# Performance work log

Measured on AMD Instinct MI355X. Metric: run time of the kernel, lower is better.

## Reference

```python
import jax, jax.numpy as jnp
import numpy as np

B = 128          # graphs per batch
NPG = 512        # nodes per graph
N = B * NPG      # 65536 nodes
E = 262144       # edges, avg degree 4, intra-graph only
IN_FEATS = 128
EDGE_FEATS = 32
EMB = 64
HEADS = 4
HC = EMB * HEADS  # 256
L = 3


def setup_inputs():
    ki = iter(jax.random.split(jax.random.key(0), 64))

    def nrm(shape):
        return jax.random.normal(next(ki), shape, jnp.float32)

    def lin(fan_in, shape):
        return jax.random.uniform(next(ki), shape, jnp.float32, -1.0, 1.0) / np.float32(np.sqrt(fan_in))

    x = nrm((N, IN_FEATS))
    edge_attr = nrm((E, EDGE_FEATS))
    g = jnp.arange(E) // (E // B)  # each edge stays inside its graph
    src = g * NPG + jax.random.randint(next(ki), (E,), 0, NPG)
    dst = g * NPG + jax.random.randint(next(ki), (E,), 0, NPG)
    edge_index = jnp.stack([src, dst]).astype(jnp.int32)
    batch_index = (jnp.arange(N) // NPG).astype(jnp.int32)
    d = dict(x=x, edge_attr=edge_attr, edge_index=edge_index, batch_index=batch_index)
    d['Wq1'] = lin(IN_FEATS, (IN_FEATS, HC)); d['bq1'] = lin(IN_FEATS, (HC,))
    d['Wk1'] = lin(IN_FEATS, (IN_FEATS, HC)); d['bk1'] = lin(IN_FEATS, (HC,))
    d['Wv1'] = lin(IN_FEATS, (IN_FEATS, HC)); d['bv1'] = lin(IN_FEATS, (HC,))
    d['We1'] = lin(EDGE_FEATS, (EDGE_FEATS, HC))
    d['Wskip1'] = lin(IN_FEATS, (IN_FEATS, HC)); d['bskip1'] = lin(IN_FEATS, (HC,))
    d['Wbeta1'] = lin(3 * HC, (3 * HC,))
    d['Wt1'] = lin(HC, (HC, EMB)); d['bt1'] = lin(HC, (EMB,))
    d['bng1'] = jnp.ones((EMB,), jnp.float32); d['bnb1'] = jnp.zeros((EMB,), jnp.float32)
    d['Wq'] = lin(EMB, (L, EMB, HC)); d['bq'] = lin(EMB, (L, HC))
    d['Wk'] = lin(EMB, (L, EMB, HC)); d['bk'] = lin(EMB, (L, HC))
    d['Wv'] = lin(EMB, (L, EMB, HC)); d['bv'] = lin(EMB, (L, HC))
    d['We'] = lin(EDGE_FEATS, (L, EDGE_FEATS, HC))
    d['Wskip'] = lin(EMB, (L, EMB, HC)); d['bskip'] = lin(EMB, (L, HC))
    d['Wbeta'] = lin(3 * HC, (L, 3 * HC))
    d['Wt'] = lin(HC, (L, HC, EMB)); d['bt'] = lin(HC, (L, EMB))
    d['bng'] = jnp.ones((L, EMB), jnp.float32); d['bnb'] = jnp.zeros((L, EMB), jnp.float32)
    d['pw0'] = lin(EMB, (EMB,)); d['pw2'] = lin(EMB, (EMB,))
    return d


def _tconv(x, src, dst, eattr, emask, Wq, bq, Wk, bk, Wv, bv, We, Wskip, bskip, Wbeta, n):
    # PyG TransformerConv (concat=True, beta=True, edge_dim), dropout off (eval)
    q = (x @ Wq + bq).reshape(n, HEADS, EMB)
    k = (x @ Wk + bk).reshape(n, HEADS, EMB)
    v = (x @ Wv + bv).reshape(n, HEADS, EMB)
    e = (eattr @ We).reshape(-1, HEADS, EMB)
    alpha = jnp.einsum('ehc,ehc->eh', q[dst], k[src] + e) / (EMB ** 0.5)
    alpha = jnp.where(emask[:, None], alpha, -jnp.inf)
    m = jax.ops.segment_max(alpha, dst, num_segments=n)
    m = jnp.where(jnp.isfinite(m), m, 0.0)
    p = jnp.where(emask[:, None], jnp.exp(alpha - m[dst]), 0.0)
    den = jax.ops.segment_sum(p, dst, num_segments=n)
    p = p / jnp.maximum(den, 1e-16)[dst]
    out = jax.ops.segment_sum((v[src] + e) * p[:, :, None], dst, num_segments=n).reshape(n, HC)
    xr = x @ Wskip + bskip
    beta = jax.nn.sigmoid(jnp.concatenate([out, xr, out - xr], axis=-1) @ Wbeta)[:, None]
    return beta * xr + (1.0 - beta) * out


def _bn(x, g, b):
    mu = x.mean(0)
    var = jnp.mean((x - mu) ** 2, 0)
    return (x - mu) / jnp.sqrt(var + 1e-5) * g + b


def _topk(x, src, dst, emask, w, npg, k_keep):
    # PyG TopKPooling: score = tanh(x.w / |w|), keep top ratio per graph, scale kept x by score
    n_graphs = x.shape[0] // npg
    score = jnp.tanh((x @ w) / jnp.linalg.norm(w))
    sv, idx = jax.lax.top_k(score.reshape(n_graphs, npg), k_keep)
    perm = (idx + jnp.arange(n_graphs)[:, None] * npg).reshape(-1)
    x_new = x[perm] * sv.reshape(-1)[:, None]
    new_idx = jnp.full(n_graphs * npg, -1, jnp.int32).at[perm].set(
        jnp.arange(n_graphs * k_keep, dtype=jnp.int32))
    sn, dn = new_idx[src], new_idx[dst]
    valid = emask & (sn >= 0) & (dn >= 0)
    return x_new, jnp.where(valid, sn, 0), jnp.where(valid, dn, 0), valid


def _forward(x, edge_attr, edge_index, batch_index, Wq1, bq1, Wk1, bk1, Wv1, bv1,
             We1, Wskip1, bskip1, Wbeta1, Wt1, bt1, bng1, bnb1,
             Wq, bq, Wk, bk, Wv, bv, We, Wskip, bskip, Wbeta, Wt, bt, bng, bnb,
             pw0, pw2):
    src, dst = edge_index[0], edge_index[1]
    emask = jnp.ones(src.shape, dtype=bool)
    n = x.shape[0]
    npg = n // B
    x = _tconv(x, src, dst, edge_attr, emask, Wq1, bq1, Wk1, bk1, Wv1, bv1,
               We1, Wskip1, bskip1, Wbeta1, n)
    x = _bn(jax.nn.relu(x @ Wt1 + bt1), bng1, bnb1)
    pool_w = {0: pw0, 2: pw2}
    greps = []
    for i in range(L):
        x = _tconv(x, src, dst, edge_attr, emask, Wq[i], bq[i], Wk[i], bk[i], Wv[i], bv[i],
                   We[i], Wskip[i], bskip[i], Wbeta[i], n)
        x = _bn(jax.nn.relu(x @ Wt[i] + bt[i]), bng[i], bnb[i])
        if i % 3 == 0 or i == L - 1:  # pooling at layers 0 and 2
            k_keep = npg // 2
            x, src, dst, emask = _topk(x, src, dst, emask, pool_w[i], npg, k_keep)
            npg = k_keep
            n = B * npg
            batch = jnp.arange(n) // npg  # pooled nodes stay contiguous per graph
            gmax = jax.ops.segment_max(x, batch, num_segments=B)
            gmean = jax.ops.segment_sum(x, batch, num_segments=B) / npg
            greps.append(jnp.concatenate([gmax, gmean], axis=-1))
    return greps[0] + greps[1]


def reference(x, edge_attr, edge_index, batch_index, Wq1, bq1, Wk1, bk1, Wv1, bv1,
              We1, Wskip1, bskip1, Wbeta1, Wt1, bt1, bng1, bnb1,
              Wq, bq, Wk, bk, Wv, bv, We, Wskip, bskip, Wbeta, Wt, bt, bng, bnb,
              pw0, pw2):
    return _forward(x, edge_attr, edge_index, batch_index, Wq1, bq1, Wk1, bk1, Wv1, bv1,
                    We1, Wskip1, bskip1, Wbeta1, Wt1, bt1, bng1, bnb1,
                    Wq, bq, Wk, bk, Wv, bv, We, Wskip, bskip, Wbeta, Wt, bt, bng, bnb,
                    pw0, pw2)
```

## Files before the change

kernel.cpp:

```cpp
#include <hip/hip_runtime.h>
#include <hip/hip_bf16.h>

#define NGRAPH 128
#define NTOT   65536
#define NE     262144
#define EPG    2048
#define HC     256

typedef __hip_bfloat16 bf16;

__device__ __forceinline__ float4 f4fma(float a, float4 b, float4 c){
  return make_float4(fmaf(a,b.x,c.x), fmaf(a,b.y,c.y), fmaf(a,b.z,c.z), fmaf(a,b.w,c.w));
}
__device__ __forceinline__ float4 f4add(float4 a, float4 b){
  return make_float4(a.x+b.x, a.y+b.y, a.z+b.z, a.w+b.w);
}

template<int F>
__global__ __launch_bounds__(256)
void gemm_qkvs_kernel(const float* __restrict__ X,
                      const float* __restrict__ W0, const float* __restrict__ B0,
                      const float* __restrict__ W1, const float* __restrict__ B1,
                      const float* __restrict__ W2, const float* __restrict__ B2,
                      const float* __restrict__ W3, const float* __restrict__ B3,
                      float* __restrict__ Y, long ystride)
{
  const int s = blockIdx.y;
  const float* __restrict__ W = (s==0)?W0:(s==1)?W1:(s==2)?W2:W3;
  const float* __restrict__ Bb= (s==0)?B0:(s==1)?B1:(s==2)?B2:B3;
  float* __restrict__ Yo = Y + (long)s*ystride;

  __shared__ __align__(16) float XsT[F][36];
  const int tid  = threadIdx.x;
  const int tcol = tid & 63;
  const int trow = tid >> 6;
  const long r0 = (long)blockIdx.x * 32;
  for (int idx = tid; idx < 32*F; idx += 256){
    int r = idx / F;
    int f = idx - r*F;
    XsT[f][r] = X[(r0 + r)*F + f];
  }
  __syncthreads();
  float4 acc[8];
#pragma unroll
  for (int r = 0; r < 8; ++r) acc[r] = make_float4(0.f,0.f,0.f,0.f);
#pragma unroll 4
  for (int f = 0; f < F; ++f){
    float4 w = *(const float4*)(&W[f*HC + 4*tcol]);
    float xs[8];
    *(float4*)&xs[0] = *(const float4*)(&XsT[f][8*trow]);
    *(float4*)&xs[4] = *(const float4*)(&XsT[f][8*trow + 4]);
#pragma unroll
    for (int r = 0; r < 8; ++r) acc[r] = f4fma(xs[r], w, acc[r]);
  }
  float4 bb = *(const float4*)(&Bb[4*tcol]);
#pragma unroll
  for (int r = 0; r < 8; ++r)
    *(float4*)(&Yo[(r0 + 8*trow + r)*HC + 4*tcol]) = f4add(acc[r], bb);
}

__global__ void mcomb_kernel(const float* __restrict__ Wq,
                             const float* __restrict__ bq,
                             const float* __restrict__ We,
                             int F, float* __restrict__ M)
{
  int id = blockIdx.x*256 + threadIdx.x;
  if (id >= (F+1)*128) return;
  int g = id >> 7;
  int j = id & 127;
  int h = j >> 5, f = j & 31;
  const float* row = (g < F) ? (Wq + (long)g*HC) : bq;
  const float* wr  = We + (long)f*HC + h*64;
  float s = 0.f;
#pragma unroll
  for (int c = 0; c < 64; ++c) s = fmaf(row[h*64 + c], wr[c], s);
  M[id] = s;
}

template<int F>
__global__ __launch_bounds__(256)
void qwe_gemm_kernel(const float* __restrict__ X, const float* __restrict__ M,
                     float* __restrict__ qwe)
{
  __shared__ __align__(16) float XsT[F][68];
  const int tid  = threadIdx.x;
  const int tcol = tid & 31;
  const int trow = tid >> 5;
  const long r0 = (long)blockIdx.x * 64;
  for (int idx = tid; idx < 64*F; idx += 256){
    int r = idx / F;
    int f = idx - r*F;
    XsT[f][r] = X[(r0 + r)*F + f];
  }
  __syncthreads();
  float4 acc[8];
#pragma unroll
  for (int r = 0; r < 8; ++r) acc[r] = make_float4(0.f,0.f,0.f,0.f);
#pragma unroll 4
  for (int f = 0; f < F; ++f){
    float4 w = *(const float4*)(&M[f*128 + 4*tcol]);
    float xs[8];
    *(float4*)&xs[0] = *(const float4*)(&XsT[f][8*trow]);
    *(float4*)&xs[4] = *(const float4*)(&XsT[f][8*trow + 4]);
#pragma unroll
    for (int r = 0; r < 8; ++r) acc[r] = f4fma(xs[r], w, acc[r]);
  }
  float4 bb = *(const float4*)(&M[F*128 + 4*tcol]);
#pragma unroll
  for (int r = 0; r < 8; ++r)
    *(float4*)(&qwe[(r0 + 8*trow + r)*128 + 4*tcol]) = f4add(acc[r], bb);
}

__global__ __launch_bounds__(256)
void csr_build_kernel(const int* __restrict__ dstA, int npgLoc,
                      int* __restrict__ eids, int* __restrict__ rowptr,
                      int* __restrict__ deg)
{
  __shared__ int dloc[2048];
  __shared__ int ord[2048];
  __shared__ int cnt[512];
  __shared__ int base[512];
  const int g = blockIdx.x, tid = threadIdx.x;
  const int ebase = g*2048;
  const int nbase = g*npgLoc;
  for (int e = tid; e < 2048; e += 256){
    int d = dstA[ebase + e];
    dloc[e] = (d >= 0) ? (d - nbase) : -1;
  }
  for (int d = tid; d < npgLoc; d += 256) cnt[d] = 0;
  __syncthreads();
  for (int r = 0; r < 8; ++r){
    const int e = r*256 + tid;
    const int d = dloc[e];
    int rk = -1;
    if (d >= 0){
      rk = cnt[d];
      for (int u = r*256; u < e; ++u)
        rk += (dloc[u] == d);
    }
    ord[e] = rk;
    __syncthreads();
    if (d >= 0) atomicAdd(&cnt[d], 1);
    __syncthreads();
  }
  if (tid == 0){
    int run = 0;
    for (int d = 0; d < npgLoc; ++d){ base[d] = run; run += cnt[d]; }
  }
  __syncthreads();
  for (int e = tid; e < 2048; e += 256){
    int d = dloc[e];
    if (d >= 0) eids[ebase + base[d] + ord[e]] = ebase + e;
  }
  for (int d = tid; d < npgLoc; d += 256){
    rowptr[nbase + d] = ebase + base[d];
    deg   [nbase + d] = cnt[d];
  }
}

__global__ __launch_bounds__(256)
void attn_kernel(int nodeOff,
                 const float* q, const float* __restrict__ k,
                 const float* __restrict__ v, const float* __restrict__ skip,
                 const float* __restrict__ qwe,
                 const int* __restrict__ rowptr, const int* __restrict__ deg,
                 const int* __restrict__ eids, const int* __restrict__ srcA,
                 const float* __restrict__ EA, const float* __restrict__ We,
                 const float* __restrict__ Wb, float* xout)
{
  const int lane = threadIdx.x & 63;
  const int g16  = lane & 15;
  const int il   = blockIdx.x*4 + (threadIdx.x >> 6);
  const int i    = nodeOff + il;

  float4 q4  = *(const float4*)(&q[(long)il*HC + 4*lane]);
  float2 qw2 = *(const float2*)(&qwe[(long)il*128 + 2*lane]);

  const int p0 = rowptr[i];
  const int dg = deg[i];
  int e_l = 0, s_l = 0;
  if (lane < dg){ e_l = eids[p0 + lane]; s_l = srcA[e_l] - nodeOff; }

  float m = -__builtin_inff();
  float den = 0.f;
  float4 acc = make_float4(0.f,0.f,0.f,0.f);
  float2 wsum = make_float2(0.f,0.f);

  for (int t = 0; t < dg; ++t){
    int e, s;
    if (t < 64){ e = __shfl(e_l, t); s = __shfl(s_l, t); }
    else { e = eids[p0 + t]; s = srcA[e] - nodeOff; }
    float2 ea2 = *(const float2*)(&EA[(long)e*32 + 2*g16]);
    float4 k4  = *(const float4*)(&k[(long)s*HC + 4*lane]);
    float4 v4  = *(const float4*)(&v[(long)s*HC + 4*lane]);
    float part = q4.x*k4.x + q4.y*k4.y + q4.z*k4.z + q4.w*k4.w
               + qw2.x*ea2.x + qw2.y*ea2.y;
    part += __shfl_xor(part, 1);
    part += __shfl_xor(part, 2);
    part += __shfl_xor(part, 4);
    part += __shfl_xor(part, 8);
    float alpha = part * 0.125f;
    float nm  = fmaxf(m, alpha);
    float scl = __expf(m - nm);
    float p   = __expf(alpha - nm);
    den = den*scl + p;
    acc.x = fmaf(acc.x, scl, p*v4.x);
    acc.y = fmaf(acc.y, scl, p*v4.y);
    acc.z = fmaf(acc.z, scl, p*v4.z);
    acc.w = fmaf(acc.w, scl, p*v4.w);
    wsum.x = fmaf(wsum.x, scl, p*ea2.x);
    wsum.y = fmaf(wsum.y, scl, p*ea2.y);
    m = nm;
  }

  float4 ecorr = make_float4(0.f,0.f,0.f,0.f);
#pragma unroll
  for (int j = 0; j < 16; ++j){
    int srcl = (lane & 48) | j;
    float wx = __shfl(wsum.x, srcl);
    float wy = __shfl(wsum.y, srcl);
    float4 w0 = *(const float4*)(&We[(2*j)*HC + 4*lane]);
    float4 w1 = *(const float4*)(&We[(2*j+1)*HC + 4*lane]);
    ecorr = f4fma(wx, w0, ecorr);
    ecorr = f4fma(wy, w1, ecorr);
  }
  float inv = 1.f / fmaxf(den, 1e-16f);
  float4 o = make_float4((acc.x+ecorr.x)*inv, (acc.y+ecorr.y)*inv,
                         (acc.z+ecorr.z)*inv, (acc.w+ecorr.w)*inv);

  float4 xr  = *(const float4*)(&skip[(long)il*HC + 4*lane]);
  float4 wb1 = *(const float4*)(&Wb[4*lane]);
  float4 wb2 = *(const float4*)(&Wb[HC + 4*lane]);
  float4 wb3 = *(const float4*)(&Wb[2*HC + 4*lane]);
  float tp = o.x*wb1.x + o.y*wb1.y + o.z*wb1.z + o.w*wb1.w
           + xr.x*wb2.x + xr.y*wb2.y + xr.z*wb2.z + xr.w*wb2.w
           + (o.x-xr.x)*wb3.x + (o.y-xr.y)*wb3.y
           + (o.z-xr.z)*wb3.z + (o.w-xr.w)*wb3.w;
  tp += __shfl_xor(tp, 1);
  tp += __shfl_xor(tp, 2);
  tp += __shfl_xor(tp, 4);
  tp += __shfl_xor(tp, 8);
  tp += __shfl_xor(tp, 16);
  tp += __shfl_xor(tp, 32);
  float beta = 1.f / (1.f + __expf(-tp));
  float4 xo = make_float4(beta*xr.x + (1.f-beta)*o.x,
                          beta*xr.y + (1.f-beta)*o.y,
                          beta*xr.z + (1.f-beta)*o.z,
                          beta*xr.w + (1.f-beta)*o.w);
  *(float4*)(&xout[(long)il*HC + 4*lane]) = xo;
}

__global__ __launch_bounds__(256)
void gemm_wt_kernel(const float* __restrict__ Xa, const float* __restrict__ Wt,
                    const float* __restrict__ bt, float* __restrict__ y)
{
  __shared__ __align__(16) float XsT[64][132];
  const int tid  = threadIdx.x;
  const int tcol = tid & 15;
  const int trow = tid >> 4;
  const long r0 = (long)blockIdx.x * 128;
  float4 acc[8];
#pragma unroll
  for (int r = 0; r < 8; ++r) acc[r] = make_float4(0.f,0.f,0.f,0.f);
  for (int kc = 0; kc < 4; ++kc){
    for (int idx = tid; idx < 128*64; idx += 256){
      int r = idx >> 6;
      int f = idx & 63;
      XsT[f][r] = Xa[(r0 + r)*HC + kc*64 + f];
    }
    __syncthreads();
#pragma unroll 4
    for (int f = 0; f < 64; ++f){
      float4 w = *(const float4*)(&Wt[(kc*64 + f)*64 + 4*tcol]);
      float xs[8];
      *(float4*)&xs[0] = *(const float4*)(&XsT[f][8*trow]);
      *(float4*)&xs[4] = *(const float4*)(&XsT[f][8*trow + 4]);
#pragma unroll
      for (int r = 0; r < 8; ++r) acc[r] = f4fma(xs[r], w, acc[r]);
    }
    __syncthreads();
  }
  float4 bb = *(const float4*)(&bt[4*tcol]);
#pragma unroll
  for (int r = 0; r < 8; ++r){
    float4 o = f4add(acc[r], bb);
    o.x = fmaxf(o.x, 0.f); o.y = fmaxf(o.y, 0.f);
    o.z = fmaxf(o.z, 0.f); o.w = fmaxf(o.w, 0.f);
    *(float4*)(&y[(r0 + 8*trow + r)*64 + 4*tcol]) = o;
  }
}

__global__ __launch_bounds__(256)
void bn_stats_kernel(const float* __restrict__ y, long total4,
                     float* __restrict__ psum, float* __restrict__ psq)
{
  __shared__ float s1[256][4], s2[256][4];
  const int tid = threadIdx.x;
  float a0=0,a1=0,a2=0,a3=0,b0=0,b1=0,b2=0,b3=0;
  const float4* y4 = (const float4*)y;
  for (long j = (long)blockIdx.x*256 + tid; j < total4; j += 65536){
    float4 v = y4[j];
    a0 += v.x; b0 += v.x*v.x;
    a1 += v.y; b1 += v.y*v.y;
    a2 += v.z; b2 += v.z*v.z;
    a3 += v.w; b3 += v.w*v.w;
  }
  s1[tid][0]=a0; s1[tid][1]=a1; s1[tid][2]=a2; s1[tid][3]=a3;
  s2[tid][0]=b0; s2[tid][1]=b1; s2[tid][2]=b2; s2[tid][3]=b3;
  __syncthreads();
  if (tid < 64){
    int t0 = tid >> 2, comp = tid & 3;
    float sa = 0.f, sb = 0.f;
#pragma unroll
    for (int kk = 0; kk < 16; ++kk){
      sa += s1[t0 + 16*kk][comp];
      sb += s2[t0 + 16*kk][comp];
    }
    psum[(long)blockIdx.x*64 + tid] = sa;
    psq [(long)blockIdx.x*64 + tid] = sb;
  }
}

__global__ void bn_finalize_kernel(const float* __restrict__ psum,
                                   const float* __restrict__ psq,
                                   float n_f, float* musd)
{
  __shared__ float s1[4][64], s2[4][64];
  const int col = threadIdx.x & 63;
  const int part = threadIdx.x >> 6;
  float a = 0.f, b = 0.f;
  for (int j = part; j < 256; j += 4){
    a += psum[(long)j*64 + col];
    b += psq [(long)j*64 + col];
  }
  s1[part][col] = a; s2[part][col] = b;
  __syncthreads();
  if (threadIdx.x < 64){
    int c = threadIdx.x;
    float sa = s1[0][c] + s1[1][c] + s1[2][c] + s1[3][c];
    float sb = s2[0][c] + s2[1][c] + s2[2][c] + s2[3][c];
    float mu = sa / n_f;
    float var = sb / n_f - mu*mu;
    musd[c] = mu;
    musd[64 + c] = rsqrtf(var + 1e-5f);
  }
}

__global__ void bn_apply_kernel(float* y, const float* __restrict__ musd,
                                const float* __restrict__ g,
                                const float* __restrict__ b, long total)
{
  long i4 = ((long)blockIdx.x * 256 + threadIdx.x) * 4;
  if (i4 >= total) return;
  int c0 = (int)(i4 & 63);
  float4 yv = *(float4*)&y[i4];
  yv.x = (yv.x - musd[c0+0]) * musd[64+c0+0] * g[c0+0] + b[c0+0];
  yv.y = (yv.y - musd[c0+1]) * musd[64+c0+1] * g[c0+1] + b[c0+1];
  yv.z = (yv.z - musd[c0+2]) * musd[64+c0+2] * g[c0+2] + b[c0+2];
  yv.w = (yv.w - musd[c0+3]) * musd[64+c0+3] * g[c0+3] + b[c0+3];
  *(float4*)&y[i4] = yv;
}

__global__ __launch_bounds__(256)
void topk_kernel(const float* __restrict__ x, const float* __restrict__ pw,
                 float* __restrict__ x2, int* __restrict__ newidx,
                 int npg, int kkeep)
{
  __shared__ float sc[512];
  __shared__ float wS[64];
  const int g = blockIdx.x, tid = threadIdx.x;
  if (tid < 64) wS[tid] = pw[tid];
  __syncthreads();
  float nrm = 0.f;
#pragma unroll
  for (int c = 0; c < 64; ++c) nrm += wS[c]*wS[c];
  nrm = sqrtf(nrm);
  for (int il = tid; il < npg; il += 256){
    const float* xr = x + (long)(g*npg + il)*64;
    float d = 0.f;
    for (int c = 0; c < 64; ++c) d = fmaf(xr[c], wS[c], d);
    sc[il] = tanhf(d / nrm);
  }
  __syncthreads();
  for (int il = tid; il < npg; il += 256){
    float si = sc[il];
    int r = 0;
    for (int j = 0; j < npg; ++j){
      float sj = sc[j];
      r += (sj > si) || (sj == si && j < il);
    }
    int gi = g*npg + il;
    if (r < kkeep){
      int npos = g*kkeep + r;
      newidx[gi] = npos;
      const float4* xr4 = (const float4*)(x + (long)gi*64);
      float4* xo4 = (float4*)(x2 + (long)npos*64);
#pragma unroll
      for (int c4 = 0; c4 < 16; ++c4){
        float4 xv = xr4[c4];
        xo4[c4] = make_float4(xv.x*si, xv.y*si, xv.z*si, xv.w*si);
      }
    } else {
      newidx[gi] = -1;
    }
  }
}

__global__ void remap_kernel(const int* __restrict__ src0, const int* __restrict__ dst0,
                             const int* __restrict__ newidx,
                             int* __restrict__ src2, int* __restrict__ dst2)
{
  int e = blockIdx.x * 256 + threadIdx.x;
  int ns = newidx[src0[e]];
  int nd = newidx[dst0[e]];
  bool ok = (ns >= 0) && (nd >= 0);
  src2[e] = ok ? ns : 0;
  dst2[e] = ok ? nd : -1;
}

__global__ void gpool_kernel(const float* __restrict__ x2, int kkeep,
                             float* grep0, float* out, int mode)
{
  const int g = blockIdx.x, c = threadIdx.x;
  float mx = -__builtin_inff(), s = 0.f;
  for (int j = 0; j < kkeep; ++j){
    float vv = x2[((long)g*kkeep + j)*64 + c];
    mx = fmaxf(mx, vv);
    s += vv;
  }
  float mean = s / (float)kkeep;
  if (mode == 0){
    grep0[g*128 + c] = mx;
    grep0[g*128 + 64 + c] = mean;
  } else {
    out[g*128 + c]      = grep0[g*128 + c] + mx;
    out[g*128 + 64 + c] = grep0[g*128 + 64 + c] + mean;
  }
}

extern "C" void kernel_launch(void* const* d_in, const int* in_sizes, int n_in,
                              void* d_out, int out_size, void* d_ws, size_t ws_size,
                              hipStream_t stream)
{
  const float* x_in = (const float*)d_in[0];
  const float* EA   = (const float*)d_in[1];
  const int*   eidx = (const int*)d_in[2];
  const int*   src0 = eidx;
  const int*   dst0 = eidx + NE;

  const float* Wq1    = (const float*)d_in[4];
  const float* bq1    = (const float*)d_in[5];
  const float* Wk1    = (const float*)d_in[6];
  const float* bk1    = (const float*)d_in[7];
  const float* Wv1    = (const float*)d_in[8];
  const float* bv1    = (const float*)d_in[9];
  const float* We1    = (const float*)d_in[10];
  const float* Wskip1 = (const float*)d_in[11];
  const float* bskip1 = (const float*)d_in[12];
  const float* Wbeta1 = (const float*)d_in[13];
  const float* Wt1    = (const float*)d_in[14];
  const float* bt1    = (const float*)d_in[15];
  const float* bng1   = (const float*)d_in[16];
  const float* bnb1   = (const float*)d_in[17];
  const float* WqL    = (const float*)d_in[18];
  const float* bqL    = (const float*)d_in[19];
  const float* WkL    = (const float*)d_in[20];
  const float* bkL    = (const float*)d_in[21];
  const float* WvL    = (const float*)d_in[22];
  const float* bvL    = (const float*)d_in[23];
  const float* WeL    = (const float*)d_in[24];
  const float* WskipL = (const float*)d_in[25];
  const float* bskipL = (const float*)d_in[26];
  const float* WbetaL = (const float*)d_in[27];
  const float* WtL    = (const float*)d_in[28];
  const float* btL    = (const float*)d_in[29];
  const float* bngL   = (const float*)d_in[30];
  const float* bnbL   = (const float*)d_in[31];
  const float* pw0    = (const float*)d_in[32];
  const float* pw2    = (const float*)d_in[33];

  const size_t FIXED = 33554432ull;
  int chunks = 1;
  while (chunks < 32 && 9ull*(67108864ull/chunks)/2 + FIXED > ws_size)
    chunks <<= 1;
  const int gpc = NGRAPH / chunks;
  const size_t C = 67108864ull / chunks;
  const long CF = (long)(C / 4);

  char* wsb = (char*)d_ws;
  float* qb   = (float*)(wsb);
  float* kb   = (float*)(wsb + C);
  float* vb   = (float*)(wsb + 2*C);
  float* sk   = (float*)(wsb + 3*C);
  float* qweb = (float*)(wsb + 4*C);
  char* p = wsb + 4*C + C/2;
  auto alloc = [&](size_t bytes){ char* r = p; p += (bytes + 255) & ~255ull; return r; };
  float* y      = (float*)alloc(16777216ull);
  float* x2     = (float*)alloc(8388608ull);
  float* ps     = (float*)alloc(65536ull);
  float* pq     = (float*)alloc(65536ull);
  float* musd   = (float*)alloc(4096ull);
  float* grep0  = (float*)alloc(65536ull);
  float* Mbuf   = (float*)alloc(66304ull);
  int* newidx   = (int*)alloc(262144ull);
  int* src2     = (int*)alloc(1048576ull);
  int* dst2     = (int*)alloc(1048576ull);
  int* eidsA    = (int*)alloc(1048576ull);
  int* rowptrA  = (int*)alloc(262144ull);
  int* degA     = (int*)alloc(262144ull);
  int* eidsB    = (int*)alloc(1048576ull);
  int* rowptrB  = (int*)alloc(131072ull);
  int* degB     = (int*)alloc(131072ull);

  csr_build_kernel<<<NGRAPH, 256, 0, stream>>>(dst0, 512, eidsA, rowptrA, degA);

  {
    const int npg = 512, n = NTOT;
    mcomb_kernel<<<(129*128 + 255)/256, 256, 0, stream>>>(Wq1, bq1, We1, 128, Mbuf);
    for (int c = 0; c < chunks; ++c){
      const int nOff = c * gpc * npg;
      const int nc   = gpc * npg;
      const float* Xc = x_in + (long)nOff * 128;
      dim3 grid(nc/32, 4);
      gemm_qkvs_kernel<128><<<grid, 256, 0, stream>>>(
          Xc, Wq1, bq1, Wk1, bk1, Wv1, bv1, Wskip1, bskip1, qb, CF);
      qwe_gemm_kernel<128><<<nc/64, 256, 0, stream>>>(Xc, Mbuf, qweb);
      attn_kernel<<<nc/4, 256, 0, stream>>>(nOff, qb, kb, vb, sk, qweb,
          rowptrA, degA, eidsA, src0, EA, We1, Wbeta1, qb);
      gemm_wt_kernel<<<nc/128, 256, 0, stream>>>(qb, Wt1, bt1, y + (long)nOff*64);
    }
    bn_stats_kernel<<<256, 256, 0, stream>>>(y, (long)n*16, ps, pq);
    bn_finalize_kernel<<<1, 256, 0, stream>>>(ps, pq, (float)n, musd);
    bn_apply_kernel<<<n/16, 256, 0, stream>>>(y, musd, bng1, bnb1, (long)n*64);
  }

  for (int i = 0; i < 3; ++i){
    const int n   = (i == 0) ? NTOT : NTOT/2;
    const int npg = (i == 0) ? 512 : 256;
    const float* xin = (i == 0) ? y : ((i == 1) ? x2 : y);
    const int* rp = (i == 0) ? rowptrA : rowptrB;
    const int* dgp= (i == 0) ? degA    : degB;
    const int* ei = (i == 0) ? eidsA   : eidsB;
    const int* sA = (i == 0) ? src0    : src2;
    const float* Wq_ = WqL + (long)i*64*256;  const float* bq_ = bqL + i*256;
    const float* Wk_ = WkL + (long)i*64*256;  const float* bk_ = bkL + i*256;
    const float* Wv_ = WvL + (long)i*64*256;  const float* bv_ = bvL + i*256;
    const float* Ws_ = WskipL + (long)i*64*256; const float* bs_ = bskipL + i*256;
    const float* We_ = WeL + (long)i*32*256;
    const float* Wb_ = WbetaL + i*768;
    const float* Wt_ = WtL + (long)i*256*64;  const float* bt_ = btL + i*64;
    const float* g_  = bngL + i*64;           const float* b_  = bnbL + i*64;

    mcomb_kernel<<<(65*128 + 255)/256, 256, 0, stream>>>(Wq_, bq_, We_, 64, Mbuf);
    for (int c = 0; c < chunks; ++c){
      const int nOff = c * gpc * npg;
      const int nc   = gpc * npg;
      const float* Xc = xin + (long)nOff * 64;
      dim3 grid(nc/32, 4);
      gemm_qkvs_kernel<64><<<grid, 256, 0, stream>>>(
          Xc, Wq_, bq_, Wk_, bk_, Wv_, bv_, Ws_, bs_, qb, CF);
      qwe_gemm_kernel<64><<<nc/64, 256, 0, stream>>>(Xc, Mbuf, qweb);
      attn_kernel<<<nc/4, 256, 0, stream>>>(nOff, qb, kb, vb, sk, qweb,
          rp, dgp, ei, sA, EA, We_, Wb_, qb);
      gemm_wt_kernel<<<nc/128, 256, 0, stream>>>(qb, Wt_, bt_, y + (long)nOff*64);
    }
    bn_stats_kernel<<<256, 256, 0, stream>>>(y, (long)n*16, ps, pq);
    bn_finalize_kernel<<<1, 256, 0, stream>>>(ps, pq, (float)n, musd);
    bn_apply_kernel<<<n/16, 256, 0, stream>>>(y, musd, g_, b_, (long)n*64);

    if (i == 0){
      topk_kernel<<<NGRAPH, 256, 0, stream>>>(y, pw0, x2, newidx, 512, 256);
      remap_kernel<<<NE/256, 256, 0, stream>>>(src0, dst0, newidx, src2, dst2);
      csr_build_kernel<<<NGRAPH, 256, 0, stream>>>(dst2, 256, eidsB, rowptrB, degB);
      gpool_kernel<<<NGRAPH, 64, 0, stream>>>(x2, 256, grep0, (float*)d_out, 0);
    } else if (i == 2){
      topk_kernel<<<NGRAPH, 256, 0, stream>>>(y, pw2, x2, newidx, 256, 128);
      gpool_kernel<<<NGRAPH, 64, 0, stream>>>(x2, 128, grep0, (float*)d_out, 1);
    }
  }

  (void)in_sizes; (void)n_in; (void)out_size; (void)ws_size;
}
```

Baseline: 1.572 ms.

## Fold q·We GEMM into QKVS GEMM and fuse BN stats into Wt GEMM

The separate qwe GEMM kernel is removed. The combined matrix M is padded to 256 columns and handled as a fifth slice (blockIdx.y=4) of the fused QKVS GEMM, which writes qwe into the qweb slot with HC stride. The Wt GEMM epilogue now reduces per-block column sums and squared sums into partial buffers, so the separate BN stats pass that re-read y is dropped, and finalize sums over n/128 blocks. The cost is double the qwe memory footprint and zero-padded wasted FLOPs in the fifth slice.

```diff
diff --git a/kernel.cpp b/kernel.cpp
--- a/kernel.cpp
+++ b/kernel.cpp
@@ -23,11 +23,12 @@
                       const float* __restrict__ W1, const float* __restrict__ B1,
                       const float* __restrict__ W2, const float* __restrict__ B2,
                       const float* __restrict__ W3, const float* __restrict__ B3,
+                      const float* __restrict__ W4, const float* __restrict__ B4,
                       float* __restrict__ Y, long ystride)
 {
   const int s = blockIdx.y;
-  const float* __restrict__ W = (s==0)?W0:(s==1)?W1:(s==2)?W2:W3;
-  const float* __restrict__ Bb= (s==0)?B0:(s==1)?B1:(s==2)?B2:B3;
+  const float* __restrict__ W = (s==0)?W0:(s==1)?W1:(s==2)?W2:(s==3)?W3:W4;
+  const float* __restrict__ Bb= (s==0)?B0:(s==1)?B1:(s==2)?B2:(s==3)?B3:B4;
   float* __restrict__ Yo = Y + (long)s*ystride;
 
   __shared__ __align__(16) float XsT[F][36];
@@ -65,50 +66,18 @@
                              int F, float* __restrict__ M)
 {
   int id = blockIdx.x*256 + threadIdx.x;
-  if (id >= (F+1)*128) return;
-  int g = id >> 7;
-  int j = id & 127;
-  int h = j >> 5, f = j & 31;
-  const float* row = (g < F) ? (Wq + (long)g*HC) : bq;
-  const float* wr  = We + (long)f*HC + h*64;
+  if (id >= (F+1)*256) return;
+  int g = id >> 8;
+  int j = id & 255;
   float s = 0.f;
-#pragma unroll
-  for (int c = 0; c < 64; ++c) s = fmaf(row[h*64 + c], wr[c], s);
+  if (j < 128){
+    int h = j >> 5, f = j & 31;
+    const float* row = (g < F) ? (Wq + (long)g*HC) : bq;
+    const float* wr  = We + (long)f*HC + h*64;
+#pragma unroll
+    for (int c = 0; c < 64; ++c) s = fmaf(row[h*64 + c], wr[c], s);
+  }
   M[id] = s;
-}
-
-template<int F>
-__global__ __launch_bounds__(256)
-void qwe_gemm_kernel(const float* __restrict__ X, const float* __restrict__ M,
-                     float* __restrict__ qwe)
-{
-  __shared__ __align__(16) float XsT[F][68];
-  const int tid  = threadIdx.x;
-  const int tcol = tid & 31;
-  const int trow = tid >> 5;
-  const long r0 = (long)blockIdx.x * 64;
-  for (int idx = tid; idx < 64*F; idx += 256){
-    int r = idx / F;
-    int f = idx - r*F;
-    XsT[f][r] = X[(r0 + r)*F + f];
-  }
-  __syncthreads();
-  float4 acc[8];
-#pragma unroll
-  for (int r = 0; r < 8; ++r) acc[r] = make_float4(0.f,0.f,0.f,0.f);
-#pragma unroll 4
-  for (int f = 0; f < F; ++f){
-    float4 w = *(const float4*)(&M[f*128 + 4*tcol]);
-    float xs[8];
-    *(float4*)&xs[0] = *(const float4*)(&XsT[f][8*trow]);
-    *(float4*)&xs[4] = *(const float4*)(&XsT[f][8*trow + 4]);
-#pragma unroll
-    for (int r = 0; r < 8; ++r) acc[r] = f4fma(xs[r], w, acc[r]);
-  }
-  float4 bb = *(const float4*)(&M[F*128 + 4*tcol]);
-#pragma unroll
-  for (int r = 0; r < 8; ++r)
-    *(float4*)(&qwe[(r0 + 8*trow + r)*128 + 4*tcol]) = f4add(acc[r], bb);
 }
 
 __global__ __launch_bounds__(256)
@@ -174,7 +143,7 @@
   const int i    = nodeOff + il;
 
   float4 q4  = *(const float4*)(&q[(long)il*HC + 4*lane]);
-  float2 qw2 = *(const float2*)(&qwe[(long)il*128 + 2*lane]);
+  float2 qw2 = *(const float2*)(&qwe[(long)il*HC + 2*lane]);
 
   const int p0 = rowptr[i];
   const int dg = deg[i];
@@ -252,7 +221,8 @@
 
 __global__ __launch_bounds__(256)
 void gemm_wt_kernel(const float* __restrict__ Xa, const float* __restrict__ Wt,
-                    const float* __restrict__ bt, float* __restrict__ y)
+                    const float* __restrict__ bt, float* __restrict__ y,
+                    float* __restrict__ psum, float* __restrict__ psq, int blkBase)
 {
   __shared__ __align__(16) float XsT[64][132];
   const int tid  = threadIdx.x;
@@ -281,55 +251,43 @@
     __syncthreads();
   }
   float4 bb = *(const float4*)(&bt[4*tcol]);
+  float4 ls = make_float4(0.f,0.f,0.f,0.f);
+  float4 lq = make_float4(0.f,0.f,0.f,0.f);
 #pragma unroll
   for (int r = 0; r < 8; ++r){
     float4 o = f4add(acc[r], bb);
     o.x = fmaxf(o.x, 0.f); o.y = fmaxf(o.y, 0.f);
     o.z = fmaxf(o.z, 0.f); o.w = fmaxf(o.w, 0.f);
     *(float4*)(&y[(r0 + 8*trow + r)*64 + 4*tcol]) = o;
-  }
-}
-
-__global__ __launch_bounds__(256)
-void bn_stats_kernel(const float* __restrict__ y, long total4,
-                     float* __restrict__ psum, float* __restrict__ psq)
-{
-  __shared__ float s1[256][4], s2[256][4];
-  const int tid = threadIdx.x;
-  float a0=0,a1=0,a2=0,a3=0,b0=0,b1=0,b2=0,b3=0;
-  const float4* y4 = (const float4*)y;
-  for (long j = (long)blockIdx.x*256 + tid; j < total4; j += 65536){
-    float4 v = y4[j];
-    a0 += v.x; b0 += v.x*v.x;
-    a1 += v.y; b1 += v.y*v.y;
-    a2 += v.z; b2 += v.z*v.z;
-    a3 += v.w; b3 += v.w*v.w;
-  }
-  s1[tid][0]=a0; s1[tid][1]=a1; s1[tid][2]=a2; s1[tid][3]=a3;
-  s2[tid][0]=b0; s2[tid][1]=b1; s2[tid][2]=b2; s2[tid][3]=b3;
+    ls.x += o.x; ls.y += o.y; ls.z += o.z; ls.w += o.w;
+    lq.x += o.x*o.x; lq.y += o.y*o.y; lq.z += o.z*o.z; lq.w += o.w*o.w;
+  }
+  float* s1 = &XsT[0][0];
+  float* s2 = s1 + 1024;
+  *(float4*)&s1[trow*64 + 4*tcol] = ls;
+  *(float4*)&s2[trow*64 + 4*tcol] = lq;
   __syncthreads();
   if (tid < 64){
-    int t0 = tid >> 2, comp = tid & 3;
-    float sa = 0.f, sb = 0.f;
-#pragma unroll
-    for (int kk = 0; kk < 16; ++kk){
-      sa += s1[t0 + 16*kk][comp];
-      sb += s2[t0 + 16*kk][comp];
-    }
-    psum[(long)blockIdx.x*64 + tid] = sa;
-    psq [(long)blockIdx.x*64 + tid] = sb;
+    float a = 0.f, b = 0.f;
+#pragma unroll
+    for (int t = 0; t < 16; ++t){
+      a += s1[t*64 + tid];
+      b += s2[t*64 + tid];
+    }
+    psum[(long)(blkBase + blockIdx.x)*64 + tid] = a;
+    psq [(long)(blkBase + blockIdx.x)*64 + tid] = b;
   }
 }
 
 __global__ void bn_finalize_kernel(const float* __restrict__ psum,
                                    const float* __restrict__ psq,
-                                   float n_f, float* musd)
+                                   int nblocks, float n_f, float* musd)
 {
   __shared__ float s1[4][64], s2[4][64];
   const int col = threadIdx.x & 63;
   const int part = threadIdx.x >> 6;
   float a = 0.f, b = 0.f;
-  for (int j = part; j < 256; j += 4){
+  for (int j = part; j < nblocks; j += 4){
     a += psum[(long)j*64 + col];
     b += psq [(long)j*64 + col];
   }
@@ -481,7 +439,7 @@
 
   const size_t FIXED = 33554432ull;
   int chunks = 1;
-  while (chunks < 32 && 9ull*(67108864ull/chunks)/2 + FIXED > ws_size)
+  while (chunks < 32 && 5ull*(67108864ull/chunks) + FIXED > ws_size)
     chunks <<= 1;
   const int gpc = NGRAPH / chunks;
   const size_t C = 67108864ull / chunks;
@@ -493,15 +451,15 @@
   float* vb   = (float*)(wsb + 2*C);
   float* sk   = (float*)(wsb + 3*C);
   float* qweb = (float*)(wsb + 4*C);
-  char* p = wsb + 4*C + C/2;
+  char* p = wsb + 5*C;
   auto alloc = [&](size_t bytes){ char* r = p; p += (bytes + 255) & ~255ull; return r; };
   float* y      = (float*)alloc(16777216ull);
   float* x2     = (float*)alloc(8388608ull);
-  float* ps     = (float*)alloc(65536ull);
-  float* pq     = (float*)alloc(65536ull);
+  float* ps     = (float*)alloc(131072ull);
+  float* pq     = (float*)alloc(131072ull);
   float* musd   = (float*)alloc(4096ull);
   float* grep0  = (float*)alloc(65536ull);
-  float* Mbuf   = (float*)alloc(66304ull);
+  float* Mbuf   = (float*)alloc(132608ull);
   int* newidx   = (int*)alloc(262144ull);
   int* src2     = (int*)alloc(1048576ull);
   int* dst2     = (int*)alloc(1048576ull);
@@ -516,21 +474,21 @@
 
   {
     const int npg = 512, n = NTOT;
-    mcomb_kernel<<<(129*128 + 255)/256, 256, 0, stream>>>(Wq1, bq1, We1, 128, Mbuf);
+    mcomb_kernel<<<129, 256, 0, stream>>>(Wq1, bq1, We1, 128, Mbuf);
     for (int c = 0; c < chunks; ++c){
       const int nOff = c * gpc * npg;
       const int nc   = gpc * npg;
       const float* Xc = x_in + (long)nOff * 128;
-      dim3 grid(nc/32, 4);
+      dim3 grid(nc/32, 5);
       gemm_qkvs_kernel<128><<<grid, 256, 0, stream>>>(
-          Xc, Wq1, bq1, Wk1, bk1, Wv1, bv1, Wskip1, bskip1, qb, CF);
-      qwe_gemm_kernel<128><<<nc/64, 256, 0, stream>>>(Xc, Mbuf, qweb);
+          Xc, Wq1, bq1, Wk1, bk1, Wv1, bv1, Wskip1, bskip1,
+          Mbuf, Mbuf + 128*256, qb, CF);
       attn_kernel<<<nc/4, 256, 0, stream>>>(nOff, qb, kb, vb, sk, qweb,
           rowptrA, degA, eidsA, src0, EA, We1, Wbeta1, qb);
-      gemm_wt_kernel<<<nc/128, 256, 0, stream>>>(qb, Wt1, bt1, y + (long)nOff*64);
-    }
-    bn_stats_kernel<<<256, 256, 0, stream>>>(y, (long)n*16, ps, pq);
-    bn_finalize_kernel<<<1, 256, 0, stream>>>(ps, pq, (float)n, musd);
+      gemm_wt_kernel<<<nc/128, 256, 0, stream>>>(qb, Wt1, bt1,
+          y + (long)nOff*64, ps, pq, nOff/128);
+    }
+    bn_finalize_kernel<<<1, 256, 0, stream>>>(ps, pq, n/128, (float)n, musd);
     bn_apply_kernel<<<n/16, 256, 0, stream>>>(y, musd, bng1, bnb1, (long)n*64);
   }
 
@@ -551,21 +509,21 @@
     const float* Wt_ = WtL + (long)i*256*64;  const float* bt_ = btL + i*64;
     const float* g_  = bngL + i*64;           const float* b_  = bnbL + i*64;
 
-    mcomb_kernel<<<(65*128 + 255)/256, 256, 0, stream>>>(Wq_, bq_, We_, 64, Mbuf);
+    mcomb_kernel<<<65, 256, 0, stream>>>(Wq_, bq_, We_, 64, Mbuf);
     for (int c = 0; c < chunks; ++c){
       const int nOff = c * gpc * npg;
       const int nc   = gpc * npg;
       const float* Xc = xin + (long)nOff * 64;
-      dim3 grid(nc/32, 4);
+      dim3 grid(nc/32, 5);
       gemm_qkvs_kernel<64><<<grid, 256, 0, stream>>>(
-          Xc, Wq_, bq_, Wk_, bk_, Wv_, bv_, Ws_, bs_, qb, CF);
-      qwe_gemm_kernel<64><<<nc/64, 256, 0, stream>>>(Xc, Mbuf, qweb);
+          Xc, Wq_, bq_, Wk_, bk_, Wv_, bv_, Ws_, bs_,
+          Mbuf, Mbuf + 64*256, qb, CF);
       attn_kernel<<<nc/4, 256, 0, stream>>>(nOff, qb, kb, vb, sk, qweb,
           rp, dgp, ei, sA, EA, We_, Wb_, qb);
-      gemm_wt_kernel<<<nc/128, 256, 0, stream>>>(qb, Wt_, bt_, y + (long)nOff*64);
-    }
-    bn_stats_kernel<<<256, 256, 0, stream>>>(y, (long)n*16, ps, pq);
-    bn_finalize_kernel<<<1, 256, 0, stream>>>(ps, pq, (float)n, musd);
+      gemm_wt_kernel<<<nc/128, 256, 0, stream>>>(qb, Wt_, bt_,
+          y + (long)nOff*64, ps, pq, nOff/128);
+    }
+    bn_finalize_kernel<<<1, 256, 0, stream>>>(ps, pq, n/128, (float)n, musd);
     bn_apply_kernel<<<n/16, 256, 0, stream>>>(y, musd, g_, b_, (long)n*64);
 
     if (i == 0){
```

Result: no change. 1.576 ms (+0.2%).
